# Performance work log

Hardware: AMD Instinct MI355X
Metric: run time of the kernel (lower is better)

## Reference

```python
import jax, jax.numpy as jnp
import numpy as np

N = 50000
E = 800000
IN_C = 128
HID = 64
HEADS = 4
NEG_SLOPE = 0.2
EPS = 1e-16


def setup_inputs() -> dict:
    key = jax.random.key(0)
    ks = jax.random.split(key, 12)
    x = jax.random.normal(ks[0], (N, IN_C), dtype=jnp.float32)
    edge_index = jax.random.randint(ks[1], (2, E), 0, N, dtype=jnp.int64)
    # layer 1: in -> (HEADS, HID), concat heads
    W1 = jax.random.normal(ks[2], (IN_C, HEADS * HID), dtype=jnp.float32) * (1.0 / np.sqrt(IN_C))
    a_src1 = jax.random.normal(ks[3], (HEADS, HID), dtype=jnp.float32) * 0.1
    a_dst1 = jax.random.normal(ks[4], (HEADS, HID), dtype=jnp.float32) * 0.1
    b1 = jnp.zeros((HEADS * HID,), dtype=jnp.float32)
    # layer 2: HEADS*HID -> (1, HID)
    W2 = jax.random.normal(ks[5], (HEADS * HID, HID), dtype=jnp.float32) * (1.0 / np.sqrt(HEADS * HID))
    a_src2 = jax.random.normal(ks[6], (1, HID), dtype=jnp.float32) * 0.1
    a_dst2 = jax.random.normal(ks[7], (1, HID), dtype=jnp.float32) * 0.1
    b2 = jnp.zeros((HID,), dtype=jnp.float32)
    return {"x": x, "edge_index": edge_index, "W1": W1, "a_src1": a_src1,
            "a_dst1": a_dst1, "b1": b1, "W2": W2, "a_src2": a_src2,
            "a_dst2": a_dst2, "b2": b2}


def _gat_conv(x, src, dst, W, a_src, a_dst, bias, heads, ch):
    n = x.shape[0]
    h = (x @ W).reshape(n, heads, ch)                       # [N,H,C]
    alpha_s = jnp.einsum('nhc,hc->nh', h, a_src)            # [N,H]
    alpha_d = jnp.einsum('nhc,hc->nh', h, a_dst)            # [N,H]
    e = jax.nn.leaky_relu(alpha_s[src] + alpha_d[dst], NEG_SLOPE)  # [E,H]
    # segment softmax over incoming edges of each dst node
    m = jax.ops.segment_max(e, dst, num_segments=n)         # [N,H]
    ex = jnp.exp(e - m[dst])
    denom = jax.ops.segment_sum(ex, dst, num_segments=n)    # [N,H]
    alpha = ex / (denom[dst] + EPS)                         # [E,H]
    msg = h[src] * alpha[:, :, None]                        # [E,H,C]
    out = jax.ops.segment_sum(msg, dst, num_segments=n)     # [N,H,C]
    return out.reshape(n, heads * ch) + bias


def reference(x, edge_index, W1, a_src1, a_dst1, b1, W2, a_src2, a_dst2, b2):
    src = edge_index[0]
    dst = edge_index[1]
    h = _gat_conv(x, src, dst, W1, a_src1, a_dst1, b1, HEADS, HID)
    h = jax.nn.elu(h)
    h = _gat_conv(h, src, dst, W2, a_src2, a_dst2, b2, 1, HID)
    h = jax.nn.elu(h)
    return h  # [N, HID] (output_dim == hidden_channels so no final linear)
```

## Files before the change

### kernel.cpp

```cpp
#include <hip/hip_runtime.h>
#include <math.h>

#define NN 50000
#define EE 800000
#define IN_C 128
#define HID 64
#define HEADS 4
#define EEP 950000
#define SCAN_BLOCKS ((NN + 255) / 256)
#define EBLOCKS ((EE + 255) / 256)

typedef __attribute__((ext_vector_type(8))) short bf16x8;
typedef __attribute__((ext_vector_type(4))) float f32x4;

#if defined(__has_builtin)
#if __has_builtin(__builtin_amdgcn_fdot2_f32_bf16)
#define HAVE_FDOT2_BF16 1
#endif
#endif


__device__ inline unsigned short f2bf(float f) {
    unsigned u = __float_as_uint(f);
    return (unsigned short)((u + 0x7fff + ((u >> 16) & 1)) >> 16);
}
__device__ inline float bf2f(unsigned short s) {
    return __uint_as_float(((unsigned)s) << 16);
}
__device__ inline unsigned prm(unsigned a, unsigned b, unsigned sel) {
    return __builtin_amdgcn_perm(a, b, sel);
}
#ifdef HAVE_FDOT2_BF16
typedef __attribute__((ext_vector_type(2))) __bf16 bf2v;
__device__ inline float fdot2bf(unsigned h, unsigned w, float acc) {
    return __builtin_amdgcn_fdot2_f32_bf16(__builtin_bit_cast(bf2v, h),
                                           __builtin_bit_cast(bf2v, w), acc, false);
}
#else
__device__ inline float fdot2bf(unsigned h, unsigned w, float acc) {
    return acc + bf2f((unsigned short)(h & 0xffff)) * bf2f((unsigned short)(w & 0xffff))
               + bf2f((unsigned short)(h >> 16)) * bf2f((unsigned short)(w >> 16));
}
#endif

__device__ inline int wave_incl_scan(int v, int lane) {
    #pragma unroll
    for (int off = 1; off < 64; off <<= 1) {
        int t = __shfl_up(v, off);
        if (lane >= off) v += t;
    }
    return v;
}

__device__ inline int block256_excl_scan(int v, int tid, int* ws4) {
    int lane = tid & 63, wv = tid >> 6;
    int incl = wave_incl_scan(v, lane);
    if (lane == 63) ws4[wv] = incl;
    __syncthreads();
    if (tid == 0) {
        int run = 0;
        #pragma unroll
        for (int i = 0; i < 4; i++) { int t = ws4[i]; ws4[i] = run; run += t; }
    }
    __syncthreads();
    return incl + ws4[wv] - v;
}


__global__ void front_kernel(const int* __restrict__ ei, int* __restrict__ deg,
                             unsigned short* __restrict__ rank,
                             const float* __restrict__ W1, unsigned short* __restrict__ W1Thi,
                             unsigned short* __restrict__ W1Tlo,
                             const float* __restrict__ W2, unsigned short* __restrict__ W2Thi,
                             unsigned short* __restrict__ W2Tlo) {
    int b = blockIdx.x;
    int tid = threadIdx.x;
    if (b < EBLOCKS) {
        int i = b * 256 + tid;
        if (i < EE) rank[i] = (unsigned short)atomicAdd(&deg[ei[EE + i]], 1);
    } else if (b < EBLOCKS + 128) {
        int idx = (b - EBLOCKS) * 256 + tid;
        int r = idx >> 8, c = idx & 255;
        float v = W1[idx];
        unsigned short h = f2bf(v);
        W1Thi[c * 128 + r] = h;
        W1Tlo[c * 128 + r] = f2bf(v - bf2f(h));
    } else {
        int idx = (b - EBLOCKS - 128) * 256 + tid;
        int r = idx >> 6, c = idx & 63;
        float v = W2[idx];
        unsigned short h = f2bf(v);
        W2Thi[c * 256 + r] = h;
        W2Tlo[c * 256 + r] = f2bf(v - bf2f(h));
    }
}

__global__ void scan_fill_kernel(const int* __restrict__ deg,
                                 unsigned long long* __restrict__ desc,
                                 int* __restrict__ row_ptr,
                                 unsigned short* __restrict__ csr_src) {
    __shared__ int ws4[4];
    __shared__ int sbase;
    int b = blockIdx.x, tid = threadIdx.x;
    int idx = b * 256 + tid;
    int draw = (idx < NN) ? deg[idx] : 0;
    int d = (draw + 1) & ~1;
    int excl = block256_excl_scan(d, tid, ws4);
    if (tid == 255) {
        unsigned total = (unsigned)(excl + d);
        __threadfence();
        atomicExch(&desc[b], (1ULL << 32) | (unsigned long long)total);
    }
    if (tid < 64) {
        int sum = 0;
        int hi = b;
        while (hi > 0) {
            int lo = hi - 64; if (lo < 0) lo = 0;
            int myi = lo + tid;
            unsigned v = 0;
            if (myi < hi) {
                unsigned long long d8;
                do { d8 = atomicAdd(&desc[myi], 0ULL); } while ((d8 >> 32) == 0);
                v = (unsigned)(d8 & 0xffffffffULL);
            }
            #pragma unroll
            for (int off = 32; off; off >>= 1) v += __shfl_down(v, off);
            v = __shfl(v, 0);
            sum += (int)v;
            hi = lo;
        }
        if (tid == 0) sbase = sum;
    }
    __syncthreads();
    int gbase = sbase;
    if (idx < NN) {
        int rp = gbase + excl;
        row_ptr[idx] = rp;
        for (int p = rp + draw; p < rp + d; ++p) csr_src[p] = 0;
    }
    if (b == gridDim.x - 1 && tid == 255) row_ptr[NN] = gbase + excl + d;
}

__global__ void scatter_kernel(const int* __restrict__ ei, const unsigned short* __restrict__ rank,
                               const int* __restrict__ row_ptr, unsigned short* __restrict__ csr_src) {
    int i = blockIdx.x * blockDim.x + threadIdx.x;
    if (i < EE) {
        int d = ei[EE + i];
        csr_src[row_ptr[d] + (int)rank[i]] = (unsigned short)ei[i];
    }
}

__global__ __launch_bounds__(256) void gemm1_mfma(
        const float* __restrict__ x,
        const unsigned short* __restrict__ Bhi, const unsigned short* __restrict__ Blo,
        const float* __restrict__ a_src, const float* __restrict__ a_dst,
        unsigned short* __restrict__ h1b, float* __restrict__ as1, float* __restrict__ ad1) {
    __shared__ unsigned short Ahi[64][136];
    __shared__ unsigned short Alo[64][136];
    int tid = threadIdx.x;
    int w = tid >> 6, lane = tid & 63;
    int lq = lane >> 4, lr = lane & 15;
    int brow = blockIdx.x * 64;
    {
        int row = tid >> 2;
        int col0 = (tid & 3) * 32;
        int gr = min(brow + row, NN - 1);
        #pragma unroll
        for (int i = 0; i < 32; i += 4) {
            float4 v = *(const float4*)(x + (size_t)gr * 128 + col0 + i);
            unsigned short h0 = f2bf(v.x), h1 = f2bf(v.y), h2 = f2bf(v.z), h3 = f2bf(v.w);
            Ahi[row][col0 + i + 0] = h0; Alo[row][col0 + i + 0] = f2bf(v.x - bf2f(h0));
            Ahi[row][col0 + i + 1] = h1; Alo[row][col0 + i + 1] = f2bf(v.y - bf2f(h1));
            Ahi[row][col0 + i + 2] = h2; Alo[row][col0 + i + 2] = f2bf(v.z - bf2f(h2));
            Ahi[row][col0 + i + 3] = h3; Alo[row][col0 + i + 3] = f2bf(v.w - bf2f(h3));
        }
    }
    __syncthreads();
    f32x4 acc[4][4];
    f32x4 zf = {0.f, 0.f, 0.f, 0.f};
    #pragma unroll
    for (int mi = 0; mi < 4; mi++)
        #pragma unroll
        for (int ni = 0; ni < 4; ni++) acc[mi][ni] = zf;
    #pragma unroll
    for (int q = 0; q < 4; q++) {
        int ko = q * 32 + lq * 8;
        bf16x8 ah[4], al[4];
        #pragma unroll
        for (int mi = 0; mi < 4; mi++) {
            ah[mi] = *(const bf16x8*)(const void*)&Ahi[mi * 16 + lr][ko];
            al[mi] = *(const bf16x8*)(const void*)&Alo[mi * 16 + lr][ko];
        }
        #pragma unroll
        for (int ni = 0; ni < 4; ni++) {
            size_t bo = (size_t)(w * 64 + ni * 16 + lr) * 128 + ko;
            bf16x8 bh = *(const bf16x8*)(const void*)(Bhi + bo);
            bf16x8 bl = *(const bf16x8*)(const void*)(Blo + bo);
            #pragma unroll
            for (int mi = 0; mi < 4; mi++) {
                acc[mi][ni] = __builtin_amdgcn_mfma_f32_16x16x32_bf16(al[mi], bh, acc[mi][ni], 0, 0, 0);
                acc[mi][ni] = __builtin_amdgcn_mfma_f32_16x16x32_bf16(ah[mi], bl, acc[mi][ni], 0, 0, 0);
                acc[mi][ni] = __builtin_amdgcn_mfma_f32_16x16x32_bf16(ah[mi], bh, acc[mi][ni], 0, 0, 0);
            }
        }
    }
    float asv[4], adv[4];
    #pragma unroll
    for (int ni = 0; ni < 4; ni++) {
        asv[ni] = a_src[w * 64 + ni * 16 + lr];
        adv[ni] = a_dst[w * 64 + ni * 16 + lr];
    }
    #pragma unroll
    for (int mi = 0; mi < 4; mi++) {
        f32x4 ps = zf, pd = zf;
        #pragma unroll
        for (int ni = 0; ni < 4; ni++)
            #pragma unroll
            for (int r = 0; r < 4; r++) {
                ps[r] += acc[mi][ni][r] * asv[ni];
                pd[r] += acc[mi][ni][r] * adv[ni];
            }
        #pragma unroll
        for (int m = 1; m < 16; m <<= 1)
            #pragma unroll
            for (int r = 0; r < 4; r++) {
                ps[r] += __shfl_xor(ps[r], m);
                pd[r] += __shfl_xor(pd[r], m);
            }
        #pragma unroll
        for (int r = 0; r < 4; r++) {
            int n = brow + mi * 16 + lq * 4 + r;
            if (lr == 0 && n < NN) { as1[n * 4 + w] = ps[r]; ad1[n * 4 + w] = pd[r]; }
        }
        #pragma unroll
        for (int ni = 0; ni < 4; ni++)
            #pragma unroll
            for (int r = 0; r < 4; r++) {
                int n = brow + mi * 16 + lq * 4 + r;
                if (n < NN)
                    h1b[(size_t)n * 256 + w * 64 + ni * 16 + lr] = f2bf(acc[mi][ni][r]);
            }
    }
}

__global__ __launch_bounds__(256) void gemm2_mfma(
        const unsigned short* __restrict__ Ab,
        const unsigned short* __restrict__ Bhi, const unsigned short* __restrict__ Blo,
        const float* __restrict__ a_src, const float* __restrict__ a_dst,
        unsigned short* __restrict__ g2b, float* __restrict__ as2, float* __restrict__ ad2) {
    int tid = threadIdx.x;
    int w = tid >> 6, lane = tid & 63;
    int lq = lane >> 4, lr = lane & 15;
    int wrow = blockIdx.x * 128 + w * 32;
    f32x4 acc[2][4];
    f32x4 zf = {0.f, 0.f, 0.f, 0.f};
    #pragma unroll
    for (int mi = 0; mi < 2; mi++)
        #pragma unroll
        for (int ni = 0; ni < 4; ni++) acc[mi][ni] = zf;
    int ra = min(wrow + lr, NN - 1);
    int rb = min(wrow + 16 + lr, NN - 1);
    #pragma unroll
    for (int q = 0; q < 8; q++) {
        int ko = q * 32 + lq * 8;
        bf16x8 ah0 = *(const bf16x8*)(const void*)(Ab + (size_t)ra * 256 + ko);
        bf16x8 ah1 = *(const bf16x8*)(const void*)(Ab + (size_t)rb * 256 + ko);
        #pragma unroll
        for (int ni = 0; ni < 4; ni++) {
            size_t bo = (size_t)(ni * 16 + lr) * 256 + ko;
            bf16x8 bh = *(const bf16x8*)(const void*)(Bhi + bo);
            bf16x8 bl = *(const bf16x8*)(const void*)(Blo + bo);
            acc[0][ni] = __builtin_amdgcn_mfma_f32_16x16x32_bf16(ah0, bl, acc[0][ni], 0, 0, 0);
            acc[0][ni] = __builtin_amdgcn_mfma_f32_16x16x32_bf16(ah0, bh, acc[0][ni], 0, 0, 0);
            acc[1][ni] = __builtin_amdgcn_mfma_f32_16x16x32_bf16(ah1, bl, acc[1][ni], 0, 0, 0);
            acc[1][ni] = __builtin_amdgcn_mfma_f32_16x16x32_bf16(ah1, bh, acc[1][ni], 0, 0, 0);
        }
    }
    float asv[4], adv[4];
    #pragma unroll
    for (int ni = 0; ni < 4; ni++) {
        asv[ni] = a_src[ni * 16 + lr];
        adv[ni] = a_dst[ni * 16 + lr];
    }
    #pragma unroll
    for (int mi = 0; mi < 2; mi++) {
        f32x4 ps = zf, pd = zf;
        #pragma unroll
        for (int ni = 0; ni < 4; ni++)
            #pragma unroll
            for (int r = 0; r < 4; r++) {
                ps[r] += acc[mi][ni][r] * asv[ni];
                pd[r] += acc[mi][ni][r] * adv[ni];
            }
        #pragma unroll
        for (int m = 1; m < 16; m <<= 1)
            #pragma unroll
            for (int r = 0; r < 4; r++) {
                ps[r] += __shfl_xor(ps[r], m);
                pd[r] += __shfl_xor(pd[r], m);
            }
        #pragma unroll
        for (int r = 0; r < 4; r++) {
            int n = wrow + mi * 16 + lq * 4 + r;
            if (lr == 0 && n < NN) { as2[n] = ps[r]; ad2[n] = pd[r]; }
        }
        #pragma unroll
        for (int ni = 0; ni < 4; ni++)
            #pragma unroll
            for (int r = 0; r < 4; r++) {
                int n = wrow + mi * 16 + lq * 4 + r;
                if (n < NN)
                    g2b[(size_t)n * 64 + ni * 16 + lr] = f2bf(acc[mi][ni][r]);
            }
    }
}

__global__ __launch_bounds__(256, 4) void agg1_kernel(
        const unsigned short* __restrict__ h1b, const int* __restrict__ row_ptr,
        const int* __restrict__ deg, const unsigned short* __restrict__ csr_src,
        const float* __restrict__ as, const float* __restrict__ ad,
        const float* __restrict__ b1, unsigned short* __restrict__ h2b) {
    __shared__ unsigned ssrc32[4][32];
    __shared__ unsigned wpk[4][4][40];
    int tid = threadIdx.x;
    int wv = tid >> 6, lane = tid & 63;
    int n = blockIdx.x * 4 + wv;
    if (n >= NN) return;
    int start = row_ptr[n], end = row_ptr[n + 1];
    int real_end = start + deg[n];
    int H = lane >> 5, l5 = lane & 31;
    int h = l5 >> 3;
    int hW = lane >> 4;
    int eSub = lane & 15;
    const unsigned short* __restrict__ hp = h1b + l5 * 8;
    float adW = ad[(size_t)n * 4 + hW];
    f32x4 a0 = {0.f, 0.f, 0.f, 0.f}, a1 = {0.f, 0.f, 0.f, 0.f};
    float dsum = 0.f;
    uint4 LA0, LB0, LA1, LB1;
    unsigned wp0, wp1;
    for (int c0 = start; c0 < end; c0 += 64) {
        int m = min(64, end - c0);
        int npairs = m >> 1;
        int G = (npairs + 1) >> 1;
        if (lane < (G << 1))
            ssrc32[wv][lane] = *(const unsigned*)(const void*)(csr_src + c0 + 2 * lane);
        for (int eb = 0; eb < m; eb += 16) {
            int j = eb + eSub;
            unsigned pairw = ssrc32[wv][j >> 1];
            float x = 0.f;
            if (c0 + j < real_end) {
                int s = (int)((pairw >> ((j & 1) << 4)) & 0xffffu);
                float e = as[(size_t)s * 4 + hW] + adW;
                e = fmaxf(e, 0.f) + 0.2f * fminf(e, 0.f);
                x = __expf(e);
                dsum += x;
            }
            unsigned p = f2bf(x);
            unsigned q = (unsigned)__shfl_down((int)p, 1);
            if ((eSub & 1) == 0 && j < m) wpk[wv][hW][j >> 1] = p | (q << 16);
        }
        if ((npairs & 1) && eSub == 0) wpk[wv][hW][npairs] = 0;
        auto LD = [&](int g, uint4& A, uint4& B, unsigned& wp) {
            unsigned both = ssrc32[wv][2 * g + H];
            int ia = (int)(both & 0xffffu), ib = (int)(both >> 16);
            A = *(const uint4*)(const void*)(hp + ia * 256);
            B = *(const uint4*)(const void*)(hp + ib * 256);
            wp = wpk[wv][h][2 * g + H];
        };
        auto CMP = [&](const uint4& A, const uint4& B, unsigned wp) {
            a0.x = fdot2bf(prm(B.x, A.x, 0x05040100), wp, a0.x);
            a0.y = fdot2bf(prm(B.x, A.x, 0x07060302), wp, a0.y);
            a0.z = fdot2bf(prm(B.y, A.y, 0x05040100), wp, a0.z);
            a0.w = fdot2bf(prm(B.y, A.y, 0x07060302), wp, a0.w);
            a1.x = fdot2bf(prm(B.z, A.z, 0x05040100), wp, a1.x);
            a1.y = fdot2bf(prm(B.z, A.z, 0x07060302), wp, a1.y);
            a1.z = fdot2bf(prm(B.w, A.w, 0x05040100), wp, a1.z);
            a1.w = fdot2bf(prm(B.w, A.w, 0x07060302), wp, a1.w);
        };
        LD(0, LA0, LB0, wp0);
        if (G > 1) LD(1, LA1, LB1, wp1);
        int g = 0;
        while (true) {
            CMP(LA0, LB0, wp0);
            if (g + 2 < G) LD(g + 2, LA0, LB0, wp0);
            if (++g >= G) break;
            CMP(LA1, LB1, wp1);
            if (g + 2 < G) LD(g + 2, LA1, LB1, wp1);
            if (++g >= G) break;
        }
    }
    #pragma unroll
    for (int off = 1; off < 16; off <<= 1) dsum += __shfl_xor(dsum, off);
    float den = __shfl(dsum, ((lane & 31) >> 3) << 4);
    a0.x += __shfl_xor(a0.x, 32); a0.y += __shfl_xor(a0.y, 32);
    a0.z += __shfl_xor(a0.z, 32); a0.w += __shfl_xor(a0.w, 32);
    a1.x += __shfl_xor(a1.x, 32); a1.y += __shfl_xor(a1.y, 32);
    a1.z += __shfl_xor(a1.z, 32); a1.w += __shfl_xor(a1.w, 32);
    if (H == 0) {
        float inv = 1.f / (den + 1e-16f);
        float4 bb0 = *(const float4*)(b1 + l5 * 8);
        float4 bb1 = *(const float4*)(b1 + l5 * 8 + 4);
        float r0 = a0.x * inv + bb0.x, r1 = a0.y * inv + bb0.y;
        float r2 = a0.z * inv + bb0.z, r3 = a0.w * inv + bb0.w;
        float r4 = a1.x * inv + bb1.x, r5 = a1.y * inv + bb1.y;
        float r6 = a1.z * inv + bb1.z, r7 = a1.w * inv + bb1.w;
        r0 = r0 > 0.f ? r0 : __expf(r0) - 1.f; r1 = r1 > 0.f ? r1 : __expf(r1) - 1.f;
        r2 = r2 > 0.f ? r2 : __expf(r2) - 1.f; r3 = r3 > 0.f ? r3 : __expf(r3) - 1.f;
        r4 = r4 > 0.f ? r4 : __expf(r4) - 1.f; r5 = r5 > 0.f ? r5 : __expf(r5) - 1.f;
        r6 = r6 > 0.f ? r6 : __expf(r6) - 1.f; r7 = r7 > 0.f ? r7 : __expf(r7) - 1.f;
        uint4 st;
        st.x = (unsigned)f2bf(r0) | ((unsigned)f2bf(r1) << 16);
        st.y = (unsigned)f2bf(r2) | ((unsigned)f2bf(r3) << 16);
        st.z = (unsigned)f2bf(r4) | ((unsigned)f2bf(r5) << 16);
        st.w = (unsigned)f2bf(r6) | ((unsigned)f2bf(r7) << 16);
        *(uint4*)(void*)(h2b + (size_t)n * 256 + l5 * 8) = st;
    }
}

__global__ __launch_bounds__(256, 4) void agg2_kernel(
        const unsigned short* __restrict__ g2b, const int* __restrict__ row_ptr,
        const int* __restrict__ deg, const unsigned short* __restrict__ csr_src,
        const float* __restrict__ as, const float* __restrict__ ad,
        const float* __restrict__ b2, float* __restrict__ out) {
    __shared__ unsigned ssrc32[4][32];
    __shared__ unsigned wpk2[4][33];
    int tid = threadIdx.x;
    int wv = tid >> 6, lane = tid & 63;
    int n = blockIdx.x * 4 + wv;
    if (n >= NN) return;
    int start = row_ptr[n], end = row_ptr[n + 1];
    int real_end = start + deg[n];
    int H = lane >> 5, l5 = lane & 31;
    const unsigned short* __restrict__ gp = g2b + l5 * 2;
    float adv = ad[n];
    float ax = 0.f, ay = 0.f;
    float dsum = 0.f;
    unsigned A0, B0, w0, A1, B1, w1v;
    for (int c0 = start; c0 < end; c0 += 64) {
        int m = min(64, end - c0);
        int npairs = m >> 1;
        int G = (npairs + 1) >> 1;
        if (lane < (G << 1))
            ssrc32[wv][lane] = *(const unsigned*)(const void*)(csr_src + c0 + 2 * lane);
        float x = 0.f;
        if (c0 + lane < real_end) {
            unsigned pw = ssrc32[wv][lane >> 1];
            int s = (int)((pw >> ((lane & 1) << 4)) & 0xffffu);
            float e = as[s] + adv;
            e = fmaxf(e, 0.f) + 0.2f * fminf(e, 0.f);
            x = __expf(e);
            dsum += x;
        }
        unsigned p = f2bf(x);
        unsigned q = (unsigned)__shfl_down((int)p, 1);
        if (((lane & 1) == 0) && lane < m) wpk2[wv][lane >> 1] = p | (q << 16);
        if ((npairs & 1) && lane == 0) wpk2[wv][npairs] = 0;
        auto LD = [&](int g, unsigned& A, unsigned& B, unsigned& wp) {
            unsigned both = ssrc32[wv][2 * g + H];
            int ia = (int)(both & 0xffffu), ib = (int)(both >> 16);
            A = *(const unsigned*)(const void*)(gp + ia * 64);
            B = *(const unsigned*)(const void*)(gp + ib * 64);
            wp = wpk2[wv][2 * g + H];
        };
        auto CMP = [&](unsigned A, unsigned B, unsigned wp) {
            ax = fdot2bf(prm(B, A, 0x05040100), wp, ax);
            ay = fdot2bf(prm(B, A, 0x07060302), wp, ay);
        };
        LD(0, A0, B0, w0);
        if (G > 1) LD(1, A1, B1, w1v);
        int g = 0;
        while (true) {
            CMP(A0, B0, w0);
            if (g + 2 < G) LD(g + 2, A0, B0, w0);
            if (++g >= G) break;
            CMP(A1, B1, w1v);
            if (g + 2 < G) LD(g + 2, A1, B1, w1v);
            if (++g >= G) break;
        }
    }
    #pragma unroll
    for (int off = 32; off; off >>= 1) dsum += __shfl_down(dsum, off);
    dsum = __shfl(dsum, 0);
    ax += __shfl_xor(ax, 32);
    ay += __shfl_xor(ay, 32);
    if (H == 0) {
        float inv = 1.f / (dsum + 1e-16f);
        float2 bv = ((const float2*)b2)[l5];
        float rx = ax * inv + bv.x;
        float ry = ay * inv + bv.y;
        rx = rx > 0.f ? rx : __expf(rx) - 1.f;
        ry = ry > 0.f ? ry : __expf(ry) - 1.f;
        *(float2*)(out + (size_t)n * 64 + l5 * 2) = make_float2(rx, ry);
    }
}


extern "C" void kernel_launch(void* const* d_in, const int* in_sizes, int n_in,
                              void* d_out, int out_size, void* d_ws, size_t ws_size,
                              hipStream_t stream) {
    const float* x      = (const float*)d_in[0];
    const int*   ei     = (const int*)d_in[1];
    const float* W1     = (const float*)d_in[2];
    const float* a_src1 = (const float*)d_in[3];
    const float* a_dst1 = (const float*)d_in[4];
    const float* b1     = (const float*)d_in[5];
    const float* W2     = (const float*)d_in[6];
    const float* a_src2 = (const float*)d_in[7];
    const float* a_dst2 = (const float*)d_in[8];
    const float* b2     = (const float*)d_in[9];
    float* out = (float*)d_out;

    char* base = (char*)d_ws;
    size_t off = 0;
    auto alloc = [&](size_t bytes) -> void* {
        void* p = base + off;
        off = (off + bytes + 255) & ~(size_t)255;
        return p;
    };
    int*   deg     = (int*)alloc(NN * sizeof(int));
    unsigned long long* desc = (unsigned long long*)alloc(SCAN_BLOCKS * sizeof(unsigned long long));
    unsigned short* rank = (unsigned short*)alloc(EE * sizeof(unsigned short));
    int*   row_ptr = (int*)alloc((NN + 1) * sizeof(int));
    unsigned short* csr_src = (unsigned short*)alloc(((size_t)EEP + 16) * sizeof(unsigned short));
    unsigned short* W1Thi = (unsigned short*)alloc(256 * 128 * 2);
    unsigned short* W1Tlo = (unsigned short*)alloc(256 * 128 * 2);
    unsigned short* W2Thi = (unsigned short*)alloc(64 * 256 * 2);
    unsigned short* W2Tlo = (unsigned short*)alloc(64 * 256 * 2);
    unsigned short* h1b   = (unsigned short*)alloc((size_t)NN * 256 * 2);
    float* as1     = (float*)alloc((size_t)NN * 4 * sizeof(float));
    float* ad1     = (float*)alloc((size_t)NN * 4 * sizeof(float));
    unsigned short* h2b   = (unsigned short*)alloc((size_t)NN * 256 * 2);
    unsigned short* g2b = h1b;
    float* as2 = as1;
    float* ad2 = ad1;

    size_t clear_bytes = (size_t)((char*)(desc + SCAN_BLOCKS) - (char*)deg);
    hipMemsetAsync(deg, 0, clear_bytes, stream);

    front_kernel<<<EBLOCKS + 128 + 64, 256, 0, stream>>>(ei, deg, rank, W1, W1Thi, W1Tlo,
                                                         W2, W2Thi, W2Tlo);
    scan_fill_kernel<<<SCAN_BLOCKS, 256, 0, stream>>>(deg, desc, row_ptr, csr_src);
    scatter_kernel<<<EBLOCKS, 256, 0, stream>>>(ei, rank, row_ptr, csr_src);

    gemm1_mfma<<<(NN + 63) / 64, 256, 0, stream>>>(x, W1Thi, W1Tlo,
                                                   a_src1, a_dst1, h1b, as1, ad1);
    agg1_kernel<<<(NN + 3) / 4, 256, 0, stream>>>(h1b, row_ptr, deg, csr_src,
                                                  as1, ad1, b1, h2b);
    gemm2_mfma<<<(NN + 127) / 128, 256, 0, stream>>>(h2b, W2Thi, W2Tlo,
                                                     a_src2, a_dst2, g2b, as2, ad2);
    agg2_kernel<<<(NN + 3) / 4, 256, 0, stream>>>(g2b, row_ptr, deg, csr_src,
                                                  as2, ad2, b2, out);
}
```

Measured before the change: 287.2 us.

## Restructure layer-2 aggregation to one channel per lane with batched 8-edge gathers

Rewrites the second-layer aggregation so each of the 64 lanes owns one output channel and gathers 2-byte bf16 values per edge, replacing the half-wave split in which each lane handled two channels of alternating edge pairs. Edges are processed in unrolled groups of 8 gathers to raise memory-level parallelism, and the cross-half reduction is removed. It also drops the occupancy hint from launch bounds. The cost is narrower 16-bit loads, which can mean more load instructions per edge row. The tail loop steps by two, so an odd edge count relies on the padded CSR entry carrying zero weight.

Result: no change. 287.3 us (+0.0%).

```diff
diff --git a/kernel.cpp b/kernel.cpp
--- a/kernel.cpp
+++ b/kernel.cpp
@@ -417,81 +417,69 @@
     }
 }
 
-__global__ __launch_bounds__(256, 4) void agg2_kernel(
+__global__ __launch_bounds__(256) void agg2_kernel(
         const unsigned short* __restrict__ g2b, const int* __restrict__ row_ptr,
         const int* __restrict__ deg, const unsigned short* __restrict__ csr_src,
         const float* __restrict__ as, const float* __restrict__ ad,
         const float* __restrict__ b2, float* __restrict__ out) {
-    __shared__ unsigned ssrc32[4][32];
-    __shared__ unsigned wpk2[4][33];
+    __shared__ int      ssrc[4][64];
+    __shared__ unsigned wbf32[4][32];
     int tid = threadIdx.x;
     int wv = tid >> 6, lane = tid & 63;
     int n = blockIdx.x * 4 + wv;
     if (n >= NN) return;
     int start = row_ptr[n], end = row_ptr[n + 1];
     int real_end = start + deg[n];
-    int H = lane >> 5, l5 = lane & 31;
-    const unsigned short* __restrict__ gp = g2b + l5 * 2;
     float adv = ad[n];
-    float ax = 0.f, ay = 0.f;
-    float dsum = 0.f;
-    unsigned A0, B0, w0, A1, B1, w1v;
+    float acc = 0.f;
+    float den = 0.f;
     for (int c0 = start; c0 < end; c0 += 64) {
         int m = min(64, end - c0);
-        int npairs = m >> 1;
-        int G = (npairs + 1) >> 1;
-        if (lane < (G << 1))
-            ssrc32[wv][lane] = *(const unsigned*)(const void*)(csr_src + c0 + 2 * lane);
         float x = 0.f;
-        if (c0 + lane < real_end) {
-            unsigned pw = ssrc32[wv][lane >> 1];
-            int s = (int)((pw >> ((lane & 1) << 4)) & 0xffffu);
-            float e = as[s] + adv;
-            e = fmaxf(e, 0.f) + 0.2f * fminf(e, 0.f);
-            x = __expf(e);
-            dsum += x;
+        if (lane < m) {
+            int s = (int)csr_src[c0 + lane];
+            ssrc[wv][lane] = s;
+            if (c0 + lane < real_end) {
+                float e = as[s] + adv;
+                e = fmaxf(e, 0.f) + 0.2f * fminf(e, 0.f);
+                x = __expf(e);
+                den += x;
+            }
         }
         unsigned p = f2bf(x);
         unsigned q = (unsigned)__shfl_down((int)p, 1);
-        if (((lane & 1) == 0) && lane < m) wpk2[wv][lane >> 1] = p | (q << 16);
-        if ((npairs & 1) && lane == 0) wpk2[wv][npairs] = 0;
-        auto LD = [&](int g, unsigned& A, unsigned& B, unsigned& wp) {
-            unsigned both = ssrc32[wv][2 * g + H];
-            int ia = (int)(both & 0xffffu), ib = (int)(both >> 16);
-            A = *(const unsigned*)(const void*)(gp + ia * 64);
-            B = *(const unsigned*)(const void*)(gp + ib * 64);
-            wp = wpk2[wv][2 * g + H];
-        };
-        auto CMP = [&](unsigned A, unsigned B, unsigned wp) {
-            ax = fdot2bf(prm(B, A, 0x05040100), wp, ax);
-            ay = fdot2bf(prm(B, A, 0x07060302), wp, ay);
-        };
-        LD(0, A0, B0, w0);
-        if (G > 1) LD(1, A1, B1, w1v);
-        int g = 0;
-        while (true) {
-            CMP(A0, B0, w0);
-            if (g + 2 < G) LD(g + 2, A0, B0, w0);
-            if (++g >= G) break;
-            CMP(A1, B1, w1v);
-            if (g + 2 < G) LD(g + 2, A1, B1, w1v);
-            if (++g >= G) break;
-        }
-    }
-    #pragma unroll
-    for (int off = 32; off; off >>= 1) dsum += __shfl_down(dsum, off);
-    dsum = __shfl(dsum, 0);
-    ax += __shfl_xor(ax, 32);
-    ay += __shfl_xor(ay, 32);
-    if (H == 0) {
-        float inv = 1.f / (dsum + 1e-16f);
-        float2 bv = ((const float2*)b2)[l5];
-        float rx = ax * inv + bv.x;
-        float ry = ay * inv + bv.y;
-        rx = rx > 0.f ? rx : __expf(rx) - 1.f;
-        ry = ry > 0.f ? ry : __expf(ry) - 1.f;
-        *(float2*)(out + (size_t)n * 64 + l5 * 2) = make_float2(rx, ry);
-    }
+        if (((lane & 1) == 0) && lane < m) wbf32[wv][lane >> 1] = p | (q << 16);
+        int j = 0;
+        for (; j + 8 <= m; j += 8) {
+            int sj[8]; unsigned gj[8];
+            #pragma unroll
+            for (int u = 0; u < 8; u++) sj[u] = ssrc[wv][j + u];
+            #pragma unroll
+            for (int u = 0; u < 8; u++)
+                gj[u] = g2b[(size_t)sj[u] * 64 + lane];
+            unsigned wp01 = wbf32[wv][(j >> 1) + 0];
+            unsigned wp23 = wbf32[wv][(j >> 1) + 1];
+            unsigned wp45 = wbf32[wv][(j >> 1) + 2];
+            unsigned wp67 = wbf32[wv][(j >> 1) + 3];
+            acc = fdot2bf(prm(gj[1], gj[0], 0x05040100), wp01, acc);
+            acc = fdot2bf(prm(gj[3], gj[2], 0x05040100), wp23, acc);
+            acc = fdot2bf(prm(gj[5], gj[4], 0x05040100), wp45, acc);
+            acc = fdot2bf(prm(gj[7], gj[6], 0x05040100), wp67, acc);
+        }
+        for (; j + 2 <= m; j += 2) {
+            int s0 = ssrc[wv][j], s1 = ssrc[wv][j + 1];
+            unsigned g0 = g2b[(size_t)s0 * 64 + lane];
+            unsigned g1 = g2b[(size_t)s1 * 64 + lane];
+            unsigned wp = wbf32[wv][j >> 1];
+            acc = fdot2bf(prm(g1, g0, 0x05040100), wp, acc);
+        }
+    }
+    #pragma unroll
+    for (int off = 32; off; off >>= 1) den += __shfl_down(den, off);
+    den = __shfl(den, 0);
+    float inv = 1.f / (den + 1e-16f);
+    float r = acc * inv + b2[lane];
+    out[(size_t)n * 64 + lane] = r > 0.f ? r : __expf(r) - 1.f;
 }
 
 
```
